# Kernel optimization log

Measured on AMD Instinct MI355X. Metric: run time of the kernel, lower is better.

Reference implementation:

```python
import jax, jax.numpy as jnp
import numpy as np

N_SKILL = 50000
B = 4096          # number of (job, resume) pairs; n_job == n_resume required by the concat
E = 65536         # edges per relation (avg degree 16)
D = 1536          # embedding_dim
HID = [512, 256, 64]


def setup_inputs() -> dict:
    key = jax.random.key(0)
    ks = jax.random.split(key, 16)
    nrm = lambda k, shape, s=0.02: jax.random.normal(k, shape, dtype=jnp.float32) * s
    inp = {
        "x_skill": jax.random.normal(ks[0], (N_SKILL, D), dtype=jnp.float32),
        "x_job": jax.random.normal(ks[1], (B, D), dtype=jnp.float32),
        "x_resume": jax.random.normal(ks[2], (B, D), dtype=jnp.float32),
        "src_sj": jax.random.randint(ks[3], (E,), 0, N_SKILL),
        "dst_sj": jax.random.randint(ks[4], (E,), 0, B),
        "src_sr": jax.random.randint(ks[5], (E,), 0, N_SKILL),
        "dst_sr": jax.random.randint(ks[6], (E,), 0, B),
        "W_rel_j": nrm(ks[7], (D, D)),
        "b_rel_j": jnp.zeros((D,), jnp.float32),
        "W_root_j": nrm(ks[8], (D, D)),
        "W_rel_r": nrm(ks[9], (D, D)),
        "b_rel_r": jnp.zeros((D,), jnp.float32),
        "W_root_r": nrm(ks[10], (D, D)),
        "W1": nrm(ks[11], (2 * D, HID[0])), "b1": jnp.zeros((HID[0],), jnp.float32),
        "W2": nrm(ks[12], (HID[0], HID[1])), "b2": jnp.zeros((HID[1],), jnp.float32),
        "W3": nrm(ks[13], (HID[1], HID[2])), "b3": jnp.zeros((HID[2],), jnp.float32),
        "W4": nrm(ks[14], (HID[2], 1)), "b4": jnp.zeros((1,), jnp.float32),
    }
    return inp


def _graph_conv(x_src, x_dst, src, dst, W_rel, b_rel, W_root):
    # PyG GraphConv (aggr='add', bipartite): out = lin_rel(sum_{j in N(i)} x_j) + lin_root(x_i)
    agg = jax.ops.segment_sum(x_src[src], dst, num_segments=x_dst.shape[0])  # [B, D]
    return agg @ W_rel + b_rel + x_dst @ W_root


def reference(x_skill, x_job, x_resume, src_sj, dst_sj, src_sr, dst_sr,
              W_rel_j, b_rel_j, W_root_j, W_rel_r, b_rel_r, W_root_r,
              W1, b1, W2, b2, W3, b3, W4, b4):
    # HeteroConv: each dst node type ('job', 'resume') receives exactly one relation,
    # so the cross-relation 'mean' aggregation is the identity.
    h_job = jax.nn.relu(_graph_conv(x_skill, x_job, src_sj, dst_sj, W_rel_j, b_rel_j, W_root_j))
    h_res = jax.nn.relu(_graph_conv(x_skill, x_resume, src_sr, dst_sr, W_rel_r, b_rel_r, W_root_r))
    h = jnp.concatenate([h_job, h_res], axis=1)  # [B, 2D]
    # MLP (dropout is inference-mode identity)
    h = jax.nn.relu(h @ W1 + b1)
    h = jax.nn.relu(h @ W2 + b2)
    h = jax.nn.relu(h @ W3 + b3)
    score = (h @ W4 + b4).squeeze(-1)  # [B]
    return score
```

## Files before the change

### kernel.cpp

```cpp
#include <hip/hip_runtime.h>

#define E_EDGES 65536
#define NB 4096
#define DD 1536
#define CAP 96

typedef unsigned short u16;
typedef __bf16 bf16x8 __attribute__((ext_vector_type(8)));
typedef float f32x4 __attribute__((ext_vector_type(4)));

#define AS1(p) ((const __attribute__((address_space(1))) void*)(p))
#define AS3(p) ((__attribute__((address_space(3))) void*)(p))

#define BAR() do { __builtin_amdgcn_s_barrier(); asm volatile("" ::: "memory"); } while (0)
#define VMCNT0() asm volatile("s_waitcnt vmcnt(0)" ::: "memory")

__device__ __forceinline__ u16 f2bf(float f) {
    unsigned u = __float_as_uint(f);
    u += 0x7fffu + ((u >> 16) & 1u);
    return (u16)(u >> 16);
}


__global__ __launch_bounds__(256) void prep_kernel(
    const float* __restrict__ w0, const float* __restrict__ w1,
    const float* __restrict__ w2, const float* __restrict__ w3,
    const float* __restrict__ w4, const float* __restrict__ w5,
    u16* __restrict__ Wjt, u16* __restrict__ Wrt,
    u16* __restrict__ W1t, u16* __restrict__ W2t,
    const int* __restrict__ sj, const int* __restrict__ dj,
    const int* __restrict__ sr, const int* __restrict__ dr,
    int* __restrict__ cnt, int* __restrict__ bkt) {
    int bid = blockIdx.x;
    if (bid >= 10880) {
        int b2 = bid - 10880;
        int rel = b2 >> 8;
        int e = (b2 & 255) * 256 + threadIdx.x;
        int s = rel ? sr[e] : sj[e];
        int d = rel ? dr[e] : dj[e];
        int slot = rel * NB + d;
        int pos = atomicAdd(&cnt[slot], 1);
        if (pos < CAP) bkt[(size_t)slot * CAP + pos] = s;
        return;
    }
    const float* in; u16* out; int N, ldo, k0, nbx;
    if (bid < 9216) {
        int m = bid / 2304;
        bid = bid % 2304;
        in = (m == 0) ? w0 : (m == 1) ? w1 : (m == 2) ? w2 : w3;
        out = (m < 2) ? Wjt : Wrt;
        N = 1536; ldo = 3072; k0 = (m & 1) ? DD : 0; nbx = 48;
    } else if (bid < 10752) {
        bid -= 9216;
        in = w4; out = W1t; N = 512; ldo = 3072; k0 = 0; nbx = 16;
    } else {
        bid -= 10752;
        in = w5; out = W2t; N = 256; ldo = 512; k0 = 0; nbx = 8;
    }
    int bx = (bid % nbx) * 32;
    int by = (bid / nbx) * 32;
    __shared__ float tile[32][33];
    int tx = threadIdx.x & 31, ty = threadIdx.x >> 5;
#pragma unroll
    for (int i = 0; i < 4; ++i)
        tile[ty + i * 8][tx] = in[(size_t)(by + ty + i * 8) * N + bx + tx];
    __syncthreads();
#pragma unroll
    for (int i = 0; i < 4; ++i) {
        int n = bx + ty + i * 8;
        int k = by + tx;
        out[(size_t)n * ldo + k0 + k] = f2bf(tile[tx][ty + i * 8]);
    }
}


__global__ __launch_bounds__(128) void agg_cvt_kernel(
    const float* __restrict__ xskill, const float* __restrict__ xj, const float* __restrict__ xr,
    const int* __restrict__ bkt, const int* __restrict__ cnt,
    u16* __restrict__ Aj, u16* __restrict__ Ar) {
    int rel = blockIdx.y;
    int row = blockIdx.x;
    int t = threadIdx.x;
    const float* xd = (rel ? xr : xj) + (size_t)row * DD;
    u16* A = (rel ? Ar : Aj) + (size_t)row * (2 * DD);

    float4 v[3];
#pragma unroll
    for (int c = 0; c < 3; ++c) v[c] = *(const float4*)(xd + t * 4 + c * 512);
#pragma unroll
    for (int c = 0; c < 3; ++c) {
        ushort4 o = {f2bf(v[c].x), f2bf(v[c].y), f2bf(v[c].z), f2bf(v[c].w)};
        *(ushort4*)(A + DD + t * 4 + c * 512) = o;
    }

    int count = cnt[rel * NB + row];
    if (count > CAP) count = CAP;
    __shared__ int sidx[CAP];
    if (t < count) sidx[t] = bkt[(size_t)(rel * NB + row) * CAP + t];
    __syncthreads();

    float4 acc0[3] = {};
    float4 acc1[3] = {};
    int e = 0;
    for (; e + 2 <= count; e += 2) {
        const float* x0 = xskill + (size_t)sidx[e] * DD;
        const float* x1 = xskill + (size_t)sidx[e + 1] * DD;
        float4 u0[3], u1[3];
#pragma unroll
        for (int c = 0; c < 3; ++c) u0[c] = *(const float4*)(x0 + t * 4 + c * 512);
#pragma unroll
        for (int c = 0; c < 3; ++c) u1[c] = *(const float4*)(x1 + t * 4 + c * 512);
#pragma unroll
        for (int c = 0; c < 3; ++c) {
            acc0[c].x += u0[c].x; acc0[c].y += u0[c].y; acc0[c].z += u0[c].z; acc0[c].w += u0[c].w;
            acc1[c].x += u1[c].x; acc1[c].y += u1[c].y; acc1[c].z += u1[c].z; acc1[c].w += u1[c].w;
        }
    }
    if (e < count) {
        const float* x0 = xskill + (size_t)sidx[e] * DD;
#pragma unroll
        for (int c = 0; c < 3; ++c) {
            float4 u = *(const float4*)(x0 + t * 4 + c * 512);
            acc0[c].x += u.x; acc0[c].y += u.y; acc0[c].z += u.z; acc0[c].w += u.w;
        }
    }
#pragma unroll
    for (int c = 0; c < 3; ++c) {
        acc0[c].x += acc1[c].x; acc0[c].y += acc1[c].y;
        acc0[c].z += acc1[c].z; acc0[c].w += acc1[c].w;
    }
#pragma unroll
    for (int c = 0; c < 3; ++c) {
        ushort4 o = {f2bf(acc0[c].x), f2bf(acc0[c].y), f2bf(acc0[c].z), f2bf(acc0[c].w)};
        *(ushort4*)(A + t * 4 + c * 512) = o;
    }
}


__global__ __launch_bounds__(512, 2) void conv_gemm(
    const u16* __restrict__ Aj, const u16* __restrict__ Wjt, const float* __restrict__ bj,
    const u16* __restrict__ Ar, const u16* __restrict__ Wrt, const float* __restrict__ br,
    u16* __restrict__ C) {
    constexpr int K = 3072, NT = K / 64, LDC = 3072;
    constexpr int BUF = 28672;
    __shared__ u16 lds[2 * BUF];
    int tid = threadIdx.x;
    int lane = tid & 63;
    int w = tid >> 6;

    int P = blockIdx.x;
    int x = P & 7;
    int q = P >> 3;
    int rel = q >> 4;
    int qq = q & 15;
    long bm = (long)(2 * x + (qq & 1)) * 256;
    long bn = (long)(qq >> 1) * 192;

    const u16* A; const u16* Bt; const float* bias; long cofs;
    if (rel) { A = Ar; Bt = Wrt; bias = br; cofs = DD; }
    else     { A = Aj; Bt = Wjt; bias = bj; cofs = 0;  }

    int wm = (w >> 2) * 128;
    int wn = (w & 3) * 48;

    const int srow = lane >> 3;
    const int skf = ((lane & 7) * 8) ^ ((lane >> 3) << 3);

    auto stageA = [&](int b, long k0) {
#pragma unroll
        for (int i = 0; i < 4; ++i) {
            int g = i * 8 + w;
            const u16* gp = A + (bm + g * 8 + srow) * (long)K + k0 + skf;
            __builtin_amdgcn_global_load_lds(AS1(gp), AS3(lds + b * BUF + g * 512), 16, 0, 0);
        }
    };
    auto stageB = [&](int b, long k0) {
#pragma unroll
        for (int i = 0; i < 3; ++i) {
            int g = i * 8 + w;
            const u16* gp = Bt + (bn + g * 8 + srow) * (long)K + k0 + skf;
            __builtin_amdgcn_global_load_lds(AS1(gp), AS3(lds + b * BUF + 16384 + g * 512), 16, 0, 0);
        }
    };

    const int lrow = lane & 15;
    const int lko = (lane >> 4) * 8;
    const int rsw = (lane & 7) << 3;

    auto ldA = [&](int b, int mi, int kk) -> bf16x8 {
        return *(const bf16x8*)(lds + b * BUF + (wm + mi * 16 + lrow) * 64 + ((kk + lko) ^ rsw));
    };
    auto ldB = [&](int b, int nj, int kk) -> bf16x8 {
        return *(const bf16x8*)(lds + b * BUF + 16384 + (wn + nj * 16 + lrow) * 64 + ((kk + lko) ^ rsw));
    };

    f32x4 acc[8][3] = {};

    stageA(0, 0); stageB(0, 0);

    for (int t = 0; t < NT; ++t) {
        int b = t & 1;
        VMCNT0();
        BAR();
        if (t + 1 < NT) {
            long k1 = (long)(t + 1) * 64;
            stageA(b ^ 1, k1); stageB(b ^ 1, k1);
        }
#pragma unroll
        for (int kk = 0; kk < 64; kk += 32) {
            bf16x8 bfr[3];
#pragma unroll
            for (int nj = 0; nj < 3; ++nj) bfr[nj] = ldB(b, nj, kk);
#pragma unroll
            for (int h = 0; h < 2; ++h) {
                bf16x8 af[4];
#pragma unroll
                for (int mi = 0; mi < 4; ++mi) af[mi] = ldA(b, h * 4 + mi, kk);
                __builtin_amdgcn_s_setprio(1);
#pragma unroll
                for (int mi = 0; mi < 4; ++mi)
#pragma unroll
                    for (int nj = 0; nj < 3; ++nj)
                        acc[h * 4 + mi][nj] = __builtin_amdgcn_mfma_f32_16x16x32_bf16(af[mi], bfr[nj], acc[h * 4 + mi][nj], 0, 0, 0);
                __builtin_amdgcn_s_setprio(0);
            }
        }
    }

    int rb = (lane >> 4) * 4, cl = lane & 15;
#pragma unroll
    for (int mi = 0; mi < 8; ++mi)
#pragma unroll
        for (int nj = 0; nj < 3; ++nj) {
            long row = bm + wm + mi * 16 + rb;
            long col = bn + wn + nj * 16 + cl;
            float bb = bias[col];
#pragma unroll
            for (int r = 0; r < 4; ++r) {
                float v = fmaxf(acc[mi][nj][r] + bb, 0.f);
                C[(row + r) * (long)LDC + cofs + col] = f2bf(v);
            }
        }
}


template <int BM, bool OUT_BF16>
__global__ __launch_bounds__(256) void gemm_bias_relu(
    const u16* __restrict__ A, const u16* __restrict__ Bt, const float* __restrict__ bias,
    void* __restrict__ C, int K, int ldc) {
    constexpr int BK = 64;
    constexpr int MI = BM / 32;
    constexpr int NITER = (BM + 128) / 32;
    __shared__ u16 lA[BM * BK];
    __shared__ u16 lB[128 * BK];
    int tid = threadIdx.x;
    int lane = tid & 63;
    int w = tid >> 6;
    long bm = (long)blockIdx.x * BM;
    long bn = (long)blockIdx.y * 128;
    int wm = (w >> 1) * (BM / 2), wn = (w & 1) * 64;
    f32x4 acc[MI][4] = {};
    const int lrow = lane & 15;
    const int lko = (lane >> 4) * 8;

    for (int k0 = 0; k0 < K; k0 += BK) {
#pragma unroll
        for (int i = 0; i < NITER; ++i) {
            int chunk = i * 256 + tid;
            int row = chunk >> 3, kc = chunk & 7;
            if (row < BM) {
                const u16* g = A + (bm + row) * (long)K + k0 + kc * 8;
                __builtin_amdgcn_global_load_lds(AS1(g), AS3((char*)lA + i * 4096 + w * 1024), 16, 0, 0);
            } else {
                const u16* g = Bt + (bn + row - BM) * (long)K + k0 + kc * 8;
                __builtin_amdgcn_global_load_lds(AS1(g), AS3((char*)lB + i * 4096 + w * 1024 - BM * 128), 16, 0, 0);
            }
        }
        __syncthreads();
#pragma unroll
        for (int kk = 0; kk < BK; kk += 32) {
            bf16x8 af[MI], bfr[4];
#pragma unroll
            for (int i = 0; i < MI; ++i)
                af[i] = *(const bf16x8*)(lA + (wm + i * 16 + lrow) * BK + kk + lko);
#pragma unroll
            for (int j = 0; j < 4; ++j)
                bfr[j] = *(const bf16x8*)(lB + (wn + j * 16 + lrow) * BK + kk + lko);
#pragma unroll
            for (int i = 0; i < MI; ++i)
#pragma unroll
                for (int j = 0; j < 4; ++j)
                    acc[i][j] = __builtin_amdgcn_mfma_f32_16x16x32_bf16(af[i], bfr[j], acc[i][j], 0, 0, 0);
        }
        __syncthreads();
    }

    int rb = (lane >> 4) * 4, cl = lane & 15;
#pragma unroll
    for (int i = 0; i < MI; ++i)
#pragma unroll
        for (int j = 0; j < 4; ++j) {
            long row = bm + wm + i * 16 + rb;
            long col = bn + wn + j * 16 + cl;
            float b = bias[col];
#pragma unroll
            for (int r = 0; r < 4; ++r) {
                float v = fmaxf(acc[i][j][r] + b, 0.f);
                long o = (row + r) * (long)ldc + col;
                if (OUT_BF16)
                    ((u16*)C)[o] = f2bf(v);
                else
                    ((float*)C)[o] = v;
            }
        }
}


__global__ __launch_bounds__(256) void l34_kernel(
    const float* __restrict__ h2, const float* __restrict__ W3, const float* __restrict__ b3,
    const float* __restrict__ W4, const float* __restrict__ b4, float* __restrict__ out) {
    __shared__ float W3s[256 * 64];
    __shared__ float hbuf[4][256];
    int tid = threadIdx.x;
#pragma unroll
    for (int i = 0; i < 16; ++i)
        ((float4*)W3s)[tid + i * 256] = ((const float4*)W3)[tid + i * 256];
    __syncthreads();
    int w = tid >> 6, t = tid & 63;
    float w4t = W4[t];
    float b3t = b3[t];
    float b40 = b4[0];
    for (int rr = 0; rr < 4; ++rr) {
        int row = blockIdx.x * 16 + w * 4 + rr;
        ((float4*)hbuf[w])[t] = ((const float4*)(h2 + (size_t)row * 256))[t];
        float acc = b3t;
#pragma unroll 8
        for (int k = 0; k < 256; ++k) acc = fmaf(hbuf[w][k], W3s[k * 64 + t], acc);
        acc = fmaxf(acc, 0.f);
        float s = acc * w4t;
#pragma unroll
        for (int o = 32; o > 0; o >>= 1) s += __shfl_down(s, o);
        if (t == 0) out[row] = s + b40;
    }
}


extern "C" void kernel_launch(void* const* d_in, const int* in_sizes, int n_in,
                              void* d_out, int out_size, void* d_ws, size_t ws_size,
                              hipStream_t stream) {
    (void)in_sizes; (void)n_in; (void)out_size; (void)ws_size;
    const float* x_skill  = (const float*)d_in[0];
    const float* x_job    = (const float*)d_in[1];
    const float* x_resume = (const float*)d_in[2];
    const int* src_sj = (const int*)d_in[3];
    const int* dst_sj = (const int*)d_in[4];
    const int* src_sr = (const int*)d_in[5];
    const int* dst_sr = (const int*)d_in[6];
    const float* W_rel_j  = (const float*)d_in[7];
    const float* b_rel_j  = (const float*)d_in[8];
    const float* W_root_j = (const float*)d_in[9];
    const float* W_rel_r  = (const float*)d_in[10];
    const float* b_rel_r  = (const float*)d_in[11];
    const float* W_root_r = (const float*)d_in[12];
    const float* W1 = (const float*)d_in[13];
    const float* b1 = (const float*)d_in[14];
    const float* W2 = (const float*)d_in[15];
    const float* b2 = (const float*)d_in[16];
    const float* W3 = (const float*)d_in[17];
    const float* b3 = (const float*)d_in[18];
    const float* W4 = (const float*)d_in[19];
    const float* b4 = (const float*)d_in[20];
    float* out = (float*)d_out;

    char* p = (char*)d_ws;
    auto alloc = [&](size_t bytes) -> char* {
        char* r = p;
        p += (bytes + 255) & ~(size_t)255;
        return r;
    };
    int* cnt = (int*)alloc(2 * NB * 4);
    int* bkt = (int*)alloc((size_t)2 * NB * CAP * 4);
    u16* Aj   = (u16*)alloc((size_t)NB * 2 * DD * 2);
    u16* Ar   = (u16*)alloc((size_t)NB * 2 * DD * 2);
    u16* Wjt  = (u16*)alloc((size_t)DD * 2 * DD * 2);
    u16* Wrt  = (u16*)alloc((size_t)DD * 2 * DD * 2);
    u16* W1t  = (u16*)alloc((size_t)512 * 3072 * 2);
    u16* W2t  = (u16*)alloc((size_t)256 * 512 * 2);
    u16* hcat = (u16*)alloc((size_t)NB * 3072 * 2);
    u16* h1   = (u16*)alloc((size_t)NB * 512 * 2);
    float* h2 = (float*)alloc((size_t)NB * 256 * 4);

    hipMemsetAsync(cnt, 0, 2 * NB * 4, stream);
    prep_kernel<<<11392, 256, 0, stream>>>(W_rel_j, W_root_j, W_rel_r, W_root_r, W1, W2,
                                           Wjt, Wrt, W1t, W2t,
                                           src_sj, dst_sj, src_sr, dst_sr, cnt, bkt);
    agg_cvt_kernel<<<dim3(NB, 2), 128, 0, stream>>>(x_skill, x_job, x_resume, bkt, cnt, Aj, Ar);

    conv_gemm<<<256, 512, 0, stream>>>(Aj, Wjt, b_rel_j, Ar, Wrt, b_rel_r, hcat);
    gemm_bias_relu<64, true><<<dim3(NB / 64, 512 / 128), 256, 0, stream>>>(hcat, W1t, b1, h1, 3072, 512);
    gemm_bias_relu<64, false><<<dim3(NB / 64, 256 / 128), 256, 0, stream>>>(h1, W2t, b2, h2, 512, 256);
    l34_kernel<<<NB / 16, 256, 0, stream>>>(h2, W3, b3, W4, b4, out);
}
```

Measured before the change: 322.3 us.

## Double-buffer MLP1 GEMM with swizzled LDS and fuse MLP2 with layers 3-4

The first MLP GEMM becomes a dedicated kernel with double-buffered LDS staging, an XOR swizzle to avoid bank conflicts, and raised wave priority around the MFMA blocks. The second MLP GEMM now covers all 256 output columns per block and is fused with the layer-3/4 tail, so h2 stays in LDS instead of being written to and read back from global memory. This removes one launch and the h2 round trip. In exchange the fused kernel uses 128KB of LDS, which limits occupancy and leaves only 64 blocks for the second GEMM.

```diff
diff --git a/kernel.cpp b/kernel.cpp
--- a/kernel.cpp
+++ b/kernel.cpp
@@ -244,52 +244,141 @@
 }
 
 
-template <int BM, bool OUT_BF16>
-__global__ __launch_bounds__(256) void gemm_bias_relu(
+__global__ __launch_bounds__(256) void mlp1_kernel(
     const u16* __restrict__ A, const u16* __restrict__ Bt, const float* __restrict__ bias,
-    void* __restrict__ C, int K, int ldc) {
-    constexpr int BK = 64;
-    constexpr int MI = BM / 32;
-    constexpr int NITER = (BM + 128) / 32;
-    __shared__ u16 lA[BM * BK];
-    __shared__ u16 lB[128 * BK];
+    u16* __restrict__ C) {
+    constexpr int K = 3072, NT = K / 64, LDC = 512;
+    constexpr int BUF = 12288;
+    __shared__ u16 lds[2 * BUF];
     int tid = threadIdx.x;
     int lane = tid & 63;
     int w = tid >> 6;
-    long bm = (long)blockIdx.x * BM;
+    long bm = (long)blockIdx.x * 64;
     long bn = (long)blockIdx.y * 128;
-    int wm = (w >> 1) * (BM / 2), wn = (w & 1) * 64;
-    f32x4 acc[MI][4] = {};
+    int wm = (w >> 1) * 32, wn = (w & 1) * 64;
+
+    const int srow = lane >> 3;
+    const int skf = ((lane & 7) * 8) ^ ((lane >> 3) << 3);
+
+    auto stageA = [&](int b, long k0) {
+#pragma unroll
+        for (int i = 0; i < 2; ++i) {
+            int g = i * 4 + w;
+            const u16* gp = A + (bm + g * 8 + srow) * (long)K + k0 + skf;
+            __builtin_amdgcn_global_load_lds(AS1(gp), AS3(lds + b * BUF + g * 512), 16, 0, 0);
+        }
+    };
+    auto stageB = [&](int b, long k0) {
+#pragma unroll
+        for (int i = 0; i < 4; ++i) {
+            int g = i * 4 + w;
+            const u16* gp = Bt + (bn + g * 8 + srow) * (long)K + k0 + skf;
+            __builtin_amdgcn_global_load_lds(AS1(gp), AS3(lds + b * BUF + 4096 + g * 512), 16, 0, 0);
+        }
+    };
+
     const int lrow = lane & 15;
     const int lko = (lane >> 4) * 8;
-
-    for (int k0 = 0; k0 < K; k0 += BK) {
-#pragma unroll
-        for (int i = 0; i < NITER; ++i) {
+    const int rsw = (lane & 7) << 3;
+
+    auto ldA = [&](int b, int mi, int kk) -> bf16x8 {
+        return *(const bf16x8*)(lds + b * BUF + (wm + mi * 16 + lrow) * 64 + ((kk + lko) ^ rsw));
+    };
+    auto ldB = [&](int b, int nj, int kk) -> bf16x8 {
+        return *(const bf16x8*)(lds + b * BUF + 4096 + (wn + nj * 16 + lrow) * 64 + ((kk + lko) ^ rsw));
+    };
+
+    f32x4 acc[2][4] = {};
+
+    stageA(0, 0); stageB(0, 0);
+
+    for (int t = 0; t < NT; ++t) {
+        int b = t & 1;
+        VMCNT0();
+        BAR();
+        if (t + 1 < NT) {
+            long k1 = (long)(t + 1) * 64;
+            stageA(b ^ 1, k1); stageB(b ^ 1, k1);
+        }
+#pragma unroll
+        for (int kk = 0; kk < 64; kk += 32) {
+            bf16x8 bfr[4];
+#pragma unroll
+            for (int nj = 0; nj < 4; ++nj) bfr[nj] = ldB(b, nj, kk);
+            bf16x8 af[2];
+#pragma unroll
+            for (int mi = 0; mi < 2; ++mi) af[mi] = ldA(b, mi, kk);
+            __builtin_amdgcn_s_setprio(1);
+#pragma unroll
+            for (int mi = 0; mi < 2; ++mi)
+#pragma unroll
+                for (int nj = 0; nj < 4; ++nj)
+                    acc[mi][nj] = __builtin_amdgcn_mfma_f32_16x16x32_bf16(af[mi], bfr[nj], acc[mi][nj], 0, 0, 0);
+            __builtin_amdgcn_s_setprio(0);
+        }
+    }
+
+    int rb = (lane >> 4) * 4, cl = lane & 15;
+#pragma unroll
+    for (int mi = 0; mi < 2; ++mi)
+#pragma unroll
+        for (int nj = 0; nj < 4; ++nj) {
+            long row = bm + wm + mi * 16 + rb;
+            long col = bn + wn + nj * 16 + cl;
+            float bb = bias[col];
+#pragma unroll
+            for (int r = 0; r < 4; ++r) {
+                float v = fmaxf(acc[mi][nj][r] + bb, 0.f);
+                C[(row + r) * (long)LDC + col] = f2bf(v);
+            }
+        }
+}
+
+
+__global__ __launch_bounds__(256) void mlp2_l34_kernel(
+    const u16* __restrict__ A, const u16* __restrict__ Bt, const float* __restrict__ b2,
+    const float* __restrict__ W3, const float* __restrict__ b3,
+    const float* __restrict__ W4, const float* __restrict__ b4, float* __restrict__ out) {
+    constexpr int K = 512;
+    __shared__ char smem[131072];
+    u16*   stg = (u16*)smem;
+    float* h2s = (float*)smem;
+    float* W3s = (float*)(smem + 65536);
+    int tid = threadIdx.x;
+    int lane = tid & 63;
+    int w = tid >> 6;
+    long bm = (long)blockIdx.x * 64;
+    int wm = (w >> 1) * 32, wn = (w & 1) * 128;
+    f32x4 acc[2][8] = {};
+    const int lrow = lane & 15;
+    const int lko = (lane >> 4) * 8;
+
+    for (int k0 = 0; k0 < K; k0 += 64) {
+#pragma unroll
+        for (int i = 0; i < 10; ++i) {
             int chunk = i * 256 + tid;
             int row = chunk >> 3, kc = chunk & 7;
-            if (row < BM) {
-                const u16* g = A + (bm + row) * (long)K + k0 + kc * 8;
-                __builtin_amdgcn_global_load_lds(AS1(g), AS3((char*)lA + i * 4096 + w * 1024), 16, 0, 0);
-            } else {
-                const u16* g = Bt + (bn + row - BM) * (long)K + k0 + kc * 8;
-                __builtin_amdgcn_global_load_lds(AS1(g), AS3((char*)lB + i * 4096 + w * 1024 - BM * 128), 16, 0, 0);
-            }
+            const u16* g = (row < 64)
+                ? A  + (bm + row) * (long)K + k0 + kc * 8
+                : Bt + (long)(row - 64) * K + k0 + kc * 8;
+            __builtin_amdgcn_global_load_lds(AS1(g), AS3((char*)stg + i * 4096 + w * 1024), 16, 0, 0);
         }
         __syncthreads();
-#pragma unroll
-        for (int kk = 0; kk < BK; kk += 32) {
-            bf16x8 af[MI], bfr[4];
-#pragma unroll
-            for (int i = 0; i < MI; ++i)
-                af[i] = *(const bf16x8*)(lA + (wm + i * 16 + lrow) * BK + kk + lko);
-#pragma unroll
-            for (int j = 0; j < 4; ++j)
-                bfr[j] = *(const bf16x8*)(lB + (wn + j * 16 + lrow) * BK + kk + lko);
-#pragma unroll
-            for (int i = 0; i < MI; ++i)
-#pragma unroll
-                for (int j = 0; j < 4; ++j)
+        const u16* lA = stg;
+        const u16* lB = stg + 64 * 64;
+#pragma unroll
+        for (int kk = 0; kk < 64; kk += 32) {
+            bf16x8 af[2], bfr[8];
+#pragma unroll
+            for (int i = 0; i < 2; ++i)
+                af[i] = *(const bf16x8*)(lA + (wm + i * 16 + lrow) * 64 + kk + lko);
+#pragma unroll
+            for (int j = 0; j < 8; ++j)
+                bfr[j] = *(const bf16x8*)(lB + (wn + j * 16 + lrow) * 64 + kk + lko);
+#pragma unroll
+            for (int i = 0; i < 2; ++i)
+#pragma unroll
+                for (int j = 0; j < 8; ++j)
                     acc[i][j] = __builtin_amdgcn_mfma_f32_16x16x32_bf16(af[i], bfr[j], acc[i][j], 0, 0, 0);
         }
         __syncthreads();
@@ -297,50 +386,35 @@
 
     int rb = (lane >> 4) * 4, cl = lane & 15;
 #pragma unroll
-    for (int i = 0; i < MI; ++i)
-#pragma unroll
-        for (int j = 0; j < 4; ++j) {
-            long row = bm + wm + i * 16 + rb;
-            long col = bn + wn + j * 16 + cl;
-            float b = bias[col];
-#pragma unroll
-            for (int r = 0; r < 4; ++r) {
-                float v = fmaxf(acc[i][j][r] + b, 0.f);
-                long o = (row + r) * (long)ldc + col;
-                if (OUT_BF16)
-                    ((u16*)C)[o] = f2bf(v);
-                else
-                    ((float*)C)[o] = v;
-            }
-        }
-}
-
-
-__global__ __launch_bounds__(256) void l34_kernel(
-    const float* __restrict__ h2, const float* __restrict__ W3, const float* __restrict__ b3,
-    const float* __restrict__ W4, const float* __restrict__ b4, float* __restrict__ out) {
-    __shared__ float W3s[256 * 64];
-    __shared__ float hbuf[4][256];
-    int tid = threadIdx.x;
+    for (int i = 0; i < 2; ++i)
+#pragma unroll
+        for (int j = 0; j < 8; ++j) {
+            int row = wm + i * 16 + rb;
+            int col = wn + j * 16 + cl;
+            float bb = b2[col];
+#pragma unroll
+            for (int r = 0; r < 4; ++r)
+                h2s[(row + r) * 256 + col] = fmaxf(acc[i][j][r] + bb, 0.f);
+        }
 #pragma unroll
     for (int i = 0; i < 16; ++i)
         ((float4*)W3s)[tid + i * 256] = ((const float4*)W3)[tid + i * 256];
     __syncthreads();
-    int w = tid >> 6, t = tid & 63;
-    float w4t = W4[t];
-    float b3t = b3[t];
+
+    float w4t = W4[lane];
+    float b3t = b3[lane];
     float b40 = b4[0];
-    for (int rr = 0; rr < 4; ++rr) {
-        int row = blockIdx.x * 16 + w * 4 + rr;
-        ((float4*)hbuf[w])[t] = ((const float4*)(h2 + (size_t)row * 256))[t];
-        float acc = b3t;
+    for (int rr = 0; rr < 16; ++rr) {
+        int row = w * 16 + rr;
+        float a3 = b3t;
+        const float* hr = h2s + row * 256;
 #pragma unroll 8
-        for (int k = 0; k < 256; ++k) acc = fmaf(hbuf[w][k], W3s[k * 64 + t], acc);
-        acc = fmaxf(acc, 0.f);
-        float s = acc * w4t;
+        for (int k = 0; k < 256; ++k) a3 = fmaf(hr[k], W3s[k * 64 + lane], a3);
+        a3 = fmaxf(a3, 0.f);
+        float s = a3 * w4t;
 #pragma unroll
         for (int o = 32; o > 0; o >>= 1) s += __shfl_down(s, o);
-        if (t == 0) out[row] = s + b40;
+        if (lane == 0) out[bm + row] = s + b40;
     }
 }
 
@@ -388,7 +462,6 @@
     u16* W2t  = (u16*)alloc((size_t)256 * 512 * 2);
     u16* hcat = (u16*)alloc((size_t)NB * 3072 * 2);
     u16* h1   = (u16*)alloc((size_t)NB * 512 * 2);
-    float* h2 = (float*)alloc((size_t)NB * 256 * 4);
 
     hipMemsetAsync(cnt, 0, 2 * NB * 4, stream);
     prep_kernel<<<11392, 256, 0, stream>>>(W_rel_j, W_root_j, W_rel_r, W_root_r, W1, W2,
@@ -397,7 +470,6 @@
     agg_cvt_kernel<<<dim3(NB, 2), 128, 0, stream>>>(x_skill, x_job, x_resume, bkt, cnt, Aj, Ar);
 
     conv_gemm<<<256, 512, 0, stream>>>(Aj, Wjt, b_rel_j, Ar, Wrt, b_rel_r, hcat);
-    gemm_bias_relu<64, true><<<dim3(NB / 64, 512 / 128), 256, 0, stream>>>(hcat, W1t, b1, h1, 3072, 512);
-    gemm_bias_relu<64, false><<<dim3(NB / 64, 256 / 128), 256, 0, stream>>>(h1, W2t, b2, h2, 512, 256);
-    l34_kernel<<<NB / 16, 256, 0, stream>>>(h2, W3, b3, W4, b4, out);
-}
+    mlp1_kernel<<<dim3(NB / 64, 4), 256, 0, stream>>>(hcat, W1t, b1, h1);
+    mlp2_l34_kernel<<<NB / 64, 256, 0, stream>>>(h1, W2t, b2, W3, b3, W4, b4, out);
+}
```

Result: slower. 350.6 us (+8.8%).
